# Kernel optimization log

Hardware: AMD Instinct MI355X
Metric: run time of the kernel (lower is better)

## Reference

```python
import jax, jax.numpy as jnp
import numpy as np

B, S, J, D = 8, 512, 25, 64      # batch, seq_len, n_joints, d_model
H, DH = 8, 32                    # n_heads, d_head
IN, OUT = J * D, J * DH * H      # 1600, 6400


def setup_inputs() -> dict:
    key = jax.random.key(0)
    ks = jax.random.split(key, 5)
    sc_in = 1.0 / np.sqrt(IN)
    sc_hd = 1.0 / np.sqrt(DH * H)
    return {
        "x": jax.random.normal(ks[0], (B, S, J, D), dtype=jnp.float32),
        # weights stored [in, out] (transpose of torch Linear.weight)
        "Wq": jax.random.normal(ks[1], (IN, OUT), dtype=jnp.float32) * sc_in,
        "Wk": jax.random.normal(ks[2], (IN, OUT), dtype=jnp.float32) * sc_in,
        "Wv": jax.random.normal(ks[3], (IN, OUT), dtype=jnp.float32) * sc_in,
        "Wb": jax.random.normal(ks[4], (DH * H, D), dtype=jnp.float32) * sc_hd,
    }


def reference(x, Wq, Wk, Wv, Wb):
    b, s, j, d = x.shape
    xf = x.reshape(b, s, j * d)                      # [B,S,J*D]
    q = xf @ Wq                                      # [B,S,OUT]
    k = xf @ Wk
    v = xf @ Wv
    # single fused attention over the full J*d_head*H width, scaled by d_model
    scores = jnp.einsum("bse,bte->bst", q, k) * (d ** -0.5)  # [B,S,S]
    causal = jnp.triu(jnp.ones((s, s), dtype=bool), k=1)
    scores = jnp.where(causal[None], -jnp.inf, scores)
    attn = jax.nn.softmax(scores, axis=-1)           # [B,S,S]
    ctx = jnp.einsum("bst,bte->bse", attn, v)        # [B,S,OUT]
    ctx = ctx.reshape(b, s, j, DH * H)               # [B,S,J,dh*H]
    out = ctx @ Wb                                   # [B,S,J,D]  (dropout = eval identity)
    return out
```

## Files before the change

kernel.cpp:

```cpp
#include <hip/hip_runtime.h>

typedef float  f32x4  __attribute__((ext_vector_type(4)));
typedef __bf16 bf16x8 __attribute__((ext_vector_type(8)));
typedef __bf16 bf16x4 __attribute__((ext_vector_type(4)));

__device__ __forceinline__ void gl_lds16(const void* g, void* l) {
    __builtin_amdgcn_global_load_lds(
        (const __attribute__((address_space(1))) void*)g,
        (__attribute__((address_space(3))) void*)l, 16, 0, 0);
}

__device__ __forceinline__ int xcd_swz(int wg, int nwg) {
    int xcd = wg & 7, idx = wg >> 3;
    int q = nwg >> 3, r = nwg & 7;
    return (xcd < r ? xcd * (q + 1) : r * (q + 1) + (xcd - r) * q) + idx;
}

__global__ void split_f32(const float* __restrict__ in, __bf16* __restrict__ hi,
                          __bf16* __restrict__ lo, long n) {
    long i = ((long)blockIdx.x * blockDim.x + threadIdx.x) * 4;
    if (i >= n) return;
    float4 v = *(const float4*)&in[i];
    bf16x4 h, l;
    h[0] = (__bf16)v.x; l[0] = (__bf16)(v.x - (float)h[0]);
    h[1] = (__bf16)v.y; l[1] = (__bf16)(v.y - (float)h[1]);
    h[2] = (__bf16)v.z; l[2] = (__bf16)(v.z - (float)h[2]);
    h[3] = (__bf16)v.w; l[3] = (__bf16)(v.w - (float)h[3]);
    *(bf16x4*)&hi[i] = h;
    *(bf16x4*)&lo[i] = l;
}

__global__ void cvt_f32(const float* __restrict__ in, __bf16* __restrict__ out, long n) {
    long i = ((long)blockIdx.x * blockDim.x + threadIdx.x) * 4;
    if (i >= n) return;
    float4 v = *(const float4*)&in[i];
    bf16x4 o = {(__bf16)v.x, (__bf16)v.y, (__bf16)v.z, (__bf16)v.w};
    *(bf16x4*)&out[i] = o;
}

__global__ void copy_f32(const float* __restrict__ in, float* __restrict__ out) {
    long i = ((long)blockIdx.x * blockDim.x + threadIdx.x) * 4;
    *(float4*)&out[i] = *(const float4*)&in[i];
}

__global__ void cvt_wb(const float* __restrict__ Wb, __bf16* __restrict__ Wbt) {
    int idx = blockIdx.x * 256 + threadIdx.x;
    int k = idx >> 6, n = idx & 63;
    Wbt[n * 256 + k] = (__bf16)Wb[idx];
}

__global__ __launch_bounds__(256) void wvb_kernel(const __bf16* __restrict__ Wvbf,
                                                  const __bf16* __restrict__ Wbt,
                                                  __bf16* __restrict__ WvbT) {
    const int kb = blockIdx.x;
    const int j  = blockIdx.y;
    const int tid = threadIdx.x;
    const int w = tid >> 6, l = tid & 63;
    const long r0 = (long)kb * 64 + w * 16;
    const int lr = l & 15, lk8 = (l >> 4) * 8;
    f32x4 acc[4];
    #pragma unroll
    for (int n = 0; n < 4; ++n) acc[n] = (f32x4){0.f, 0.f, 0.f, 0.f};
    #pragma unroll
    for (int kt = 0; kt < 8; ++kt) {
        const int k = kt * 32 + lk8;
        bf16x8 a = *(const bf16x8*)&Wvbf[(r0 + lr) * 6400 + j * 256 + k];
        #pragma unroll
        for (int n = 0; n < 4; ++n) {
            bf16x8 b = *(const bf16x8*)&Wbt[(n * 16 + lr) * 256 + k];
            acc[n] = __builtin_amdgcn_mfma_f32_16x16x32_bf16(a, b, acc[n], 0, 0, 0);
        }
    }
    const int rr = (l >> 4) * 4;
    #pragma unroll
    for (int n = 0; n < 4; ++n)
        #pragma unroll
        for (int r = 0; r < 4; ++r)
            WvbT[(long)(j * 64 + n * 16 + lr) * 1600 + r0 + rr + r] = (__bf16)acc[n][r];
}

template <int OUTMODE, bool CAUSAL, bool SWZ>
__global__ __launch_bounds__(256) void gemm3f(
    const __bf16* __restrict__ Ahi, const __bf16* __restrict__ Alo,
    const __bf16* __restrict__ Bhi, const __bf16* __restrict__ Blo,
    float* __restrict__ C, __bf16* __restrict__ Ch, __bf16* __restrict__ Cl,
    int kspp, int nkc, int lda, int ldb, int ldc, int M, int N,
    long sA, long sB, long sC, float scale)
{
    __shared__ __bf16 AsH[8192], AsL[8192], BsH[8192], BsL[8192];
    int bx = blockIdx.x, by = blockIdx.y;
    if (SWZ) {
        int f = xcd_swz(by * gridDim.x + bx, gridDim.x * gridDim.y);
        bx = f % gridDim.x; by = f / gridDim.x;
    }
    const int n0 = bx * 128, m0 = by * 128;
    if (CAUSAL && n0 > m0) return;
    const int bz = blockIdx.z;
    const int batch = bz / nkc, kc = bz % nkc;
    Ahi += (long)batch * sA; Alo += (long)batch * sA;
    Bhi += (long)batch * sB; Blo += (long)batch * sB;
    const int k0base = kc * kspp * 64;

    const int tid = threadIdx.x;
    const int w = tid >> 6, l = tid & 63;
    const int wr = w >> 1, wc = w & 1;
    const int lr = l & 15;
    const int lk8 = (l >> 4) * 8;
    const int kswz = (lr & 7) << 3;
    const int srow = l >> 3;
    const int scol = ((l & 7) ^ (l >> 3)) * 8;

    f32x4 acc[4][4];
    #pragma unroll
    for (int m = 0; m < 4; ++m)
        #pragma unroll
        for (int n = 0; n < 4; ++n) acc[m][n] = (f32x4){0.f, 0.f, 0.f, 0.f};

    for (int kt = 0; kt < kspp; ++kt) {
        const int k0 = k0base + (kt << 6);
        __syncthreads();
        #pragma unroll
        for (int it = 0; it < 4; ++it) {
            const int j = it * 4 + w;
            const int grow = j * 8 + srow;
            const long ga = (long)(m0 + grow) * lda + k0 + scol;
            const long gb = (long)(n0 + grow) * ldb + k0 + scol;
            gl_lds16(Ahi + ga, &AsH[j * 512]);
            gl_lds16(Alo + ga, &AsL[j * 512]);
            gl_lds16(Bhi + gb, &BsH[j * 512]);
            gl_lds16(Blo + gb, &BsL[j * 512]);
        }
        __syncthreads();
        #pragma unroll
        for (int kk = 0; kk < 2; ++kk) {
            const int kx = (kk * 32 + lk8) ^ kswz;
            bf16x8 ah[4], bh[4], tt[4];
            #pragma unroll
            for (int m = 0; m < 4; ++m)
                ah[m] = *(const bf16x8*)&AsH[(wr * 64 + m * 16 + lr) * 64 + kx];
            #pragma unroll
            for (int n = 0; n < 4; ++n)
                bh[n] = *(const bf16x8*)&BsH[(wc * 64 + n * 16 + lr) * 64 + kx];
            #pragma unroll
            for (int m = 0; m < 4; ++m)
                #pragma unroll
                for (int n = 0; n < 4; ++n)
                    acc[m][n] = __builtin_amdgcn_mfma_f32_16x16x32_bf16(ah[m], bh[n], acc[m][n], 0, 0, 0);
            #pragma unroll
            for (int n = 0; n < 4; ++n)
                tt[n] = *(const bf16x8*)&BsL[(wc * 64 + n * 16 + lr) * 64 + kx];
            #pragma unroll
            for (int m = 0; m < 4; ++m)
                #pragma unroll
                for (int n = 0; n < 4; ++n)
                    acc[m][n] = __builtin_amdgcn_mfma_f32_16x16x32_bf16(ah[m], tt[n], acc[m][n], 0, 0, 0);
            #pragma unroll
            for (int m = 0; m < 4; ++m)
                tt[m] = *(const bf16x8*)&AsL[(wr * 64 + m * 16 + lr) * 64 + kx];
            #pragma unroll
            for (int m = 0; m < 4; ++m)
                #pragma unroll
                for (int n = 0; n < 4; ++n)
                    acc[m][n] = __builtin_amdgcn_mfma_f32_16x16x32_bf16(tt[m], bh[n], acc[m][n], 0, 0, 0);
        }
    }

    const int r0 = wr * 64 + (l >> 4) * 4;
    const int c0 = wc * 64 + lr;
    #pragma unroll
    for (int m = 0; m < 4; ++m)
        #pragma unroll
        for (int n = 0; n < 4; ++n)
            #pragma unroll
            for (int r = 0; r < 4; ++r) {
                int row = m0 + r0 + m * 16 + r;
                int col = n0 + c0 + n * 16;
                if (row < M && col < N) {
                    float v = acc[m][n][r] * scale;
                    long idx = (long)batch * sC + (long)row * ldc + col;
                    if (OUTMODE == 1) {
                        unsafeAtomicAdd(&C[idx], v);
                    } else if (OUTMODE == 2) {
                        __bf16 h = (__bf16)v;
                        Ch[idx] = h;
                        Cl[idx] = (__bf16)(v - (float)h);
                    } else {
                        C[idx] = v;
                    }
                }
            }
}

template <typename CT, bool TRANSC, bool SWZ>
__global__ __launch_bounds__(256) void gemm_bt(const __bf16* __restrict__ A,
                                               const __bf16* __restrict__ Bt,
                                               CT* __restrict__ C,
                                               int K, int lda, int ldb, int ldc,
                                               long sA, long sB, long sC,
                                               float scale, int causal, int Nlim) {
    __shared__ __bf16 As[8192];
    __shared__ __bf16 Bs[8192];
    int bx = blockIdx.x, by = blockIdx.y;
    if (SWZ) {
        int f = xcd_swz(by * gridDim.x + bx, gridDim.x * gridDim.y);
        bx = f % gridDim.x; by = f / gridDim.x;
    }
    const int n0 = bx * 128, m0 = by * 128;
    A  += (long)blockIdx.z * sA;
    Bt += (long)blockIdx.z * sB;
    int ksteps = K >> 6;
    if (causal == 2) { int lim = (m0 >> 6) + 2; if (lim < ksteps) ksteps = lim; }

    const int tid = threadIdx.x;
    const int w = tid >> 6, l = tid & 63;
    const int wr = w >> 1, wc = w & 1;
    const int lr = l & 15;
    const int lk8 = (l >> 4) * 8;
    const int kswz = (lr & 7) << 3;
    const int srow = l >> 3;
    const int scol = ((l & 7) ^ (l >> 3)) * 8;

    f32x4 acc[4][4];
    #pragma unroll
    for (int m = 0; m < 4; ++m)
        #pragma unroll
        for (int n = 0; n < 4; ++n) acc[m][n] = (f32x4){0.f, 0.f, 0.f, 0.f};

    for (int kt = 0; kt < ksteps; ++kt) {
        const int k0 = kt << 6;
        __syncthreads();
        #pragma unroll
        for (int it = 0; it < 4; ++it) {
            const int j = it * 4 + w;
            const int grow = j * 8 + srow;
            gl_lds16(A  + (long)(m0 + grow) * lda + k0 + scol, &As[j * 512]);
            gl_lds16(Bt + (long)(n0 + grow) * ldb + k0 + scol, &Bs[j * 512]);
        }
        __syncthreads();
        #pragma unroll
        for (int kk = 0; kk < 2; ++kk) {
            const int kx = (kk * 32 + lk8) ^ kswz;
            bf16x8 a[4], b[4];
            #pragma unroll
            for (int m = 0; m < 4; ++m)
                a[m] = *(const bf16x8*)&As[(wr * 64 + m * 16 + lr) * 64 + kx];
            #pragma unroll
            for (int n = 0; n < 4; ++n)
                b[n] = *(const bf16x8*)&Bs[(wc * 64 + n * 16 + lr) * 64 + kx];
            #pragma unroll
            for (int m = 0; m < 4; ++m)
                #pragma unroll
                for (int n = 0; n < 4; ++n)
                    acc[m][n] = __builtin_amdgcn_mfma_f32_16x16x32_bf16(a[m], b[n], acc[m][n], 0, 0, 0);
        }
    }

    const int r0 = m0 + wr * 64 + (l >> 4) * 4;
    const int c0 = n0 + wc * 64 + lr;
    #pragma unroll
    for (int m = 0; m < 4; ++m)
        #pragma unroll
        for (int n = 0; n < 4; ++n)
            #pragma unroll
            for (int r = 0; r < 4; ++r) {
                float v = acc[m][n][r] * scale;
                int row = r0 + m * 16 + r;
                int col = c0 + n * 16;
                if (TRANSC) {
                    C[(long)(row >> 9) * sC + (long)col * ldc + (row & 511)] = (CT)v;
                } else if (col < Nlim) {
                    C[(long)blockIdx.z * sC + (long)row * ldc + col] = (CT)v;
                }
            }
}

__global__ __launch_bounds__(256) void softmax_causal(const float* __restrict__ S,
                                                      __bf16* __restrict__ P) {
    __shared__ float red[8];
    const long rid = blockIdx.x;
    const int s = (int)(rid & 511);
    const float* row = S + rid * 512;
    __bf16* prow = P + rid * 512;
    const int t = threadIdx.x;
    float x0 = (t       <= s) ? row[t]       : -3.0e38f;
    float x1 = (t + 256 <= s) ? row[t + 256] : -3.0e38f;
    float m = fmaxf(x0, x1);
    #pragma unroll
    for (int off = 1; off < 64; off <<= 1) m = fmaxf(m, __shfl_xor(m, off));
    const int w = t >> 6;
    if ((t & 63) == 0) red[w] = m;
    __syncthreads();
    m = fmaxf(fmaxf(red[0], red[1]), fmaxf(red[2], red[3]));
    float e0 = __expf(x0 - m), e1 = __expf(x1 - m);
    float sum = e0 + e1;
    #pragma unroll
    for (int off = 1; off < 64; off <<= 1) sum += __shfl_xor(sum, off);
    if ((t & 63) == 0) red[4 + w] = sum;
    __syncthreads();
    sum = red[4] + red[5] + red[6] + red[7];
    const float rinv = 1.0f / sum;
    prow[t]       = (__bf16)(e0 * rinv);
    prow[t + 256] = (__bf16)(e1 * rinv);
}

extern "C" void kernel_launch(void* const* d_in, const int* in_sizes, int n_in,
                              void* d_out, int out_size, void* d_ws, size_t ws_size,
                              hipStream_t stream) {
    (void)in_sizes; (void)n_in; (void)out_size; (void)ws_size;
    const float* x  = (const float*)d_in[0];
    const float* Wq = (const float*)d_in[1];
    const float* Wk = (const float*)d_in[2];
    const float* Wv = (const float*)d_in[3];
    const float* Wb = (const float*)d_in[4];
    float* out = (float*)d_out;
    char* ws = (char*)d_ws;

    __bf16* Wqh = (__bf16*)(ws + 0);
    __bf16* Wql = (__bf16*)(ws + 20480000);
    __bf16* Wkh = (__bf16*)(ws + 40960000);
    __bf16* Wkl = (__bf16*)(ws + 61440000);
    float*  Gt  = (float*) (ws + 81920000);
    __bf16* Gth = (__bf16*)(ws + 92160000);
    __bf16* Gtl = (__bf16*)(ws + 97484800);
    __bf16* Wbt = (__bf16*)(ws + 102809600);
    __bf16* xh  = (__bf16*)(ws + 0);
    __bf16* xl  = (__bf16*)(ws + 13107200);
    __bf16* th  = (__bf16*)(ws + 26214400);
    __bf16* tl  = (__bf16*)(ws + 39321600);
    float*  s   = (float*) (ws + 81920000);
    __bf16* P   = (__bf16*)(ws + 90308608);
    __bf16* Wvbf = (__bf16*)(ws + 13107200);
    __bf16* WvbT = (__bf16*)(ws + 39321600);
    __bf16* VWt  = (__bf16*)(ws + 44646400);
    float*  CtxF = (float*) (ws + 0);

    split_f32<<<10000, 256, 0, stream>>>(Wq, Wqh, Wql, 10240000L);
    split_f32<<<10000, 256, 0, stream>>>(Wk, Wkh, Wkl, 10240000L);
    hipMemsetAsync(Gt, 0, 10240000, stream);
    gemm3f<1, false, true><<<dim3(13, 13, 4), 256, 0, stream>>>(
        Wkh, Wkl, Wqh, Wql, Gt, nullptr, nullptr,
        25, 4, 6400, 6400, 1600, 1600, 1600, 0L, 0L, 0L, 1.0f);
    hipMemsetAsync((char*)Gth + 5120000, 0, 204800, stream);
    hipMemsetAsync((char*)Gtl + 5120000, 0, 204800, stream);
    split_f32<<<2500, 256, 0, stream>>>(Gt, Gth, Gtl, 2560000L);

    split_f32<<<6400, 256, 0, stream>>>(x, xh, xl, 6553600L);
    gemm3f<2, false, true><<<dim3(13, 32, 1), 256, 0, stream>>>(
        xh, xl, Gth, Gtl, nullptr, th, tl,
        25, 1, 1600, 1600, 1600, 4096, 1600, 0L, 0L, 0L, 1.0f);

    hipMemsetAsync(s, 0, 8388608, stream);
    gemm3f<1, true, false><<<dim3(4, 4, 40), 256, 0, stream>>>(
        th, tl, xh, xl, s, nullptr, nullptr,
        5, 5, 1600, 1600, 512, 512, 512, 819200L, 819200L, 262144L, 0.125f);

    softmax_causal<<<4096, 256, 0, stream>>>(s, P);

    cvt_f32<<<10000, 256, 0, stream>>>(Wv, Wvbf, 10240000L);
    cvt_wb<<<64, 256, 0, stream>>>(Wb, Wbt);
    hipMemsetAsync(WvbT, 0, 5324800, stream);
    wvb_kernel<<<dim3(25, 25), 256, 0, stream>>>(Wvbf, Wbt, WvbT);

    gemm_bt<__bf16, true, true><<<dim3(13, 32), 256, 0, stream>>>(
        xh, WvbT, VWt, 1600, 1600, 1600, 512, 0L, 0L, 851968L, 1.0f, 0, 1664);

    gemm_bt<float, false, false><<<dim3(13, 4, 8), 256, 0, stream>>>(
        P, VWt, CtxF, 512, 512, 512, 1600,
        262144L, 851968L, 819200L, 1.0f, 2, 1600);

    copy_f32<<<6400, 256, 0, stream>>>(CtxF, out);
}
```

Before: 390.9 us.

## Double-buffer gemm3f LDS staging, fuse Wv conversion, halve Gram split-K

New measurement: 430.7 us. 10.2% more time.

```diff
diff --git a/kernel.cpp b/kernel.cpp
--- a/kernel.cpp
+++ b/kernel.cpp
@@ -30,14 +30,6 @@
     *(bf16x4*)&lo[i] = l;
 }
 
-__global__ void cvt_f32(const float* __restrict__ in, __bf16* __restrict__ out, long n) {
-    long i = ((long)blockIdx.x * blockDim.x + threadIdx.x) * 4;
-    if (i >= n) return;
-    float4 v = *(const float4*)&in[i];
-    bf16x4 o = {(__bf16)v.x, (__bf16)v.y, (__bf16)v.z, (__bf16)v.w};
-    *(bf16x4*)&out[i] = o;
-}
-
 __global__ void copy_f32(const float* __restrict__ in, float* __restrict__ out) {
     long i = ((long)blockIdx.x * blockDim.x + threadIdx.x) * 4;
     *(float4*)&out[i] = *(const float4*)&in[i];
@@ -49,7 +41,7 @@
     Wbt[n * 256 + k] = (__bf16)Wb[idx];
 }
 
-__global__ __launch_bounds__(256) void wvb_kernel(const __bf16* __restrict__ Wvbf,
+__global__ __launch_bounds__(256) void wvb_kernel(const float* __restrict__ Wv,
                                                   const __bf16* __restrict__ Wbt,
                                                   __bf16* __restrict__ WvbT) {
     const int kb = blockIdx.x;
@@ -64,7 +56,11 @@
     #pragma unroll
     for (int kt = 0; kt < 8; ++kt) {
         const int k = kt * 32 + lk8;
-        bf16x8 a = *(const bf16x8*)&Wvbf[(r0 + lr) * 6400 + j * 256 + k];
+        const float* ap = &Wv[(r0 + lr) * 6400 + j * 256 + k];
+        float4 f0 = *(const float4*)ap;
+        float4 f1 = *(const float4*)(ap + 4);
+        bf16x8 a = {(__bf16)f0.x, (__bf16)f0.y, (__bf16)f0.z, (__bf16)f0.w,
+                    (__bf16)f1.x, (__bf16)f1.y, (__bf16)f1.z, (__bf16)f1.w};
         #pragma unroll
         for (int n = 0; n < 4; ++n) {
             bf16x8 b = *(const bf16x8*)&Wbt[(n * 16 + lr) * 256 + k];
@@ -87,7 +83,7 @@
     int kspp, int nkc, int lda, int ldb, int ldc, int M, int N,
     long sA, long sB, long sC, float scale)
 {
-    __shared__ __bf16 AsH[8192], AsL[8192], BsH[8192], BsL[8192];
+    __shared__ __bf16 lds[2 * 4 * 8192];
     int bx = blockIdx.x, by = blockIdx.y;
     if (SWZ) {
         int f = xcd_swz(by * gridDim.x + bx, gridDim.x * gridDim.y);
@@ -116,31 +112,42 @@
         #pragma unroll
         for (int n = 0; n < 4; ++n) acc[m][n] = (f32x4){0.f, 0.f, 0.f, 0.f};
 
-    for (int kt = 0; kt < kspp; ++kt) {
+    auto STAGE = [&](int kt, int b) {
         const int k0 = k0base + (kt << 6);
-        __syncthreads();
+        __bf16* base = lds + b * 32768;
         #pragma unroll
         for (int it = 0; it < 4; ++it) {
             const int j = it * 4 + w;
             const int grow = j * 8 + srow;
             const long ga = (long)(m0 + grow) * lda + k0 + scol;
             const long gb = (long)(n0 + grow) * ldb + k0 + scol;
-            gl_lds16(Ahi + ga, &AsH[j * 512]);
-            gl_lds16(Alo + ga, &AsL[j * 512]);
-            gl_lds16(Bhi + gb, &BsH[j * 512]);
-            gl_lds16(Blo + gb, &BsL[j * 512]);
-        }
-        __syncthreads();
+            gl_lds16(Ahi + ga, base +         j * 512);
+            gl_lds16(Alo + ga, base +  8192 + j * 512);
+            gl_lds16(Bhi + gb, base + 16384 + j * 512);
+            gl_lds16(Blo + gb, base + 24576 + j * 512);
+        }
+    };
+
+    STAGE(0, 0);
+    __syncthreads();
+
+    for (int kt = 0; kt < kspp; ++kt) {
+        const int cur = kt & 1;
+        if (kt + 1 < kspp) STAGE(kt + 1, cur ^ 1);
+        const __bf16* AH = lds + cur * 32768;
+        const __bf16* AL = AH + 8192;
+        const __bf16* BH = AH + 16384;
+        const __bf16* BL = AH + 24576;
         #pragma unroll
         for (int kk = 0; kk < 2; ++kk) {
             const int kx = (kk * 32 + lk8) ^ kswz;
             bf16x8 ah[4], bh[4], tt[4];
             #pragma unroll
             for (int m = 0; m < 4; ++m)
-                ah[m] = *(const bf16x8*)&AsH[(wr * 64 + m * 16 + lr) * 64 + kx];
+                ah[m] = *(const bf16x8*)&AH[(wr * 64 + m * 16 + lr) * 64 + kx];
             #pragma unroll
             for (int n = 0; n < 4; ++n)
-                bh[n] = *(const bf16x8*)&BsH[(wc * 64 + n * 16 + lr) * 64 + kx];
+                bh[n] = *(const bf16x8*)&BH[(wc * 64 + n * 16 + lr) * 64 + kx];
             #pragma unroll
             for (int m = 0; m < 4; ++m)
                 #pragma unroll
@@ -148,7 +155,7 @@
                     acc[m][n] = __builtin_amdgcn_mfma_f32_16x16x32_bf16(ah[m], bh[n], acc[m][n], 0, 0, 0);
             #pragma unroll
             for (int n = 0; n < 4; ++n)
-                tt[n] = *(const bf16x8*)&BsL[(wc * 64 + n * 16 + lr) * 64 + kx];
+                tt[n] = *(const bf16x8*)&BL[(wc * 64 + n * 16 + lr) * 64 + kx];
             #pragma unroll
             for (int m = 0; m < 4; ++m)
                 #pragma unroll
@@ -156,13 +163,14 @@
                     acc[m][n] = __builtin_amdgcn_mfma_f32_16x16x32_bf16(ah[m], tt[n], acc[m][n], 0, 0, 0);
             #pragma unroll
             for (int m = 0; m < 4; ++m)
-                tt[m] = *(const bf16x8*)&AsL[(wr * 64 + m * 16 + lr) * 64 + kx];
+                tt[m] = *(const bf16x8*)&AL[(wr * 64 + m * 16 + lr) * 64 + kx];
             #pragma unroll
             for (int m = 0; m < 4; ++m)
                 #pragma unroll
                 for (int n = 0; n < 4; ++n)
                     acc[m][n] = __builtin_amdgcn_mfma_f32_16x16x32_bf16(tt[m], bh[n], acc[m][n], 0, 0, 0);
         }
+        __syncthreads();
     }
 
     const int r0 = wr * 64 + (l >> 4) * 4;
@@ -329,7 +337,6 @@
     __bf16* tl  = (__bf16*)(ws + 39321600);
     float*  s   = (float*) (ws + 81920000);
     __bf16* P   = (__bf16*)(ws + 90308608);
-    __bf16* Wvbf = (__bf16*)(ws + 13107200);
     __bf16* WvbT = (__bf16*)(ws + 39321600);
     __bf16* VWt  = (__bf16*)(ws + 44646400);
     float*  CtxF = (float*) (ws + 0);
@@ -337,9 +344,9 @@
     split_f32<<<10000, 256, 0, stream>>>(Wq, Wqh, Wql, 10240000L);
     split_f32<<<10000, 256, 0, stream>>>(Wk, Wkh, Wkl, 10240000L);
     hipMemsetAsync(Gt, 0, 10240000, stream);
-    gemm3f<1, false, true><<<dim3(13, 13, 4), 256, 0, stream>>>(
+    gemm3f<1, false, true><<<dim3(13, 13, 2), 256, 0, stream>>>(
         Wkh, Wkl, Wqh, Wql, Gt, nullptr, nullptr,
-        25, 4, 6400, 6400, 1600, 1600, 1600, 0L, 0L, 0L, 1.0f);
+        50, 2, 6400, 6400, 1600, 1600, 1600, 0L, 0L, 0L, 1.0f);
     hipMemsetAsync((char*)Gth + 5120000, 0, 204800, stream);
     hipMemsetAsync((char*)Gtl + 5120000, 0, 204800, stream);
     split_f32<<<2500, 256, 0, stream>>>(Gt, Gth, Gtl, 2560000L);
@@ -356,10 +363,9 @@
 
     softmax_causal<<<4096, 256, 0, stream>>>(s, P);
 
-    cvt_f32<<<10000, 256, 0, stream>>>(Wv, Wvbf, 10240000L);
     cvt_wb<<<64, 256, 0, stream>>>(Wb, Wbt);
     hipMemsetAsync(WvbT, 0, 5324800, stream);
-    wvb_kernel<<<dim3(25, 25), 256, 0, stream>>>(Wvbf, Wbt, WvbT);
+    wvb_kernel<<<dim3(25, 25), 256, 0, stream>>>(Wv, Wbt, WvbT);
 
     gemm_bt<__bf16, true, true><<<dim3(13, 32), 256, 0, stream>>>(
         xh, WvbT, VWt, 1600, 1600, 1600, 512, 0L, 0L, 851968L, 1.0f, 0, 1664);
```
